# Kernel optimization log

Hardware: AMD Instinct MI355X
Metric: run time of the kernel (lower is better)

The kernel has to match this reference:

```python
import jax, jax.numpy as jnp
import numpy as np

VOCAB = 100000
DIM = 128
B = 16384
C_MAX = 10
K_NEG = 5


def setup_inputs() -> dict:
    key = jax.random.key(0)
    k1, k2, k3, k4, k5, k6 = jax.random.split(key, 6)
    bound = 0.5 / DIM
    return {
        "target_words": jax.random.randint(k1, (B,), 0, VOCAB),
        "context_words": jax.random.randint(k2, (B, C_MAX), 0, VOCAB),
        "context_lens": jax.random.randint(k3, (B,), 0, C_MAX + 1),
        "negative_words": jax.random.randint(k4, (B, K_NEG), 0, VOCAB),
        # input embeddings init: uniform(-0.5/dim, 0.5/dim); output init zeros in the
        # original, but we use small random values so gradients/scores are non-trivial.
        "in_emb": jax.random.uniform(k5, (VOCAB, DIM), jnp.float32, -bound, bound),
        "out_emb": jax.random.normal(k6, (VOCAB, DIM), jnp.float32) * 0.01,
    }


def reference(target_words, context_words, context_lens, negative_words, in_emb, out_emb):
    t = in_emb[target_words]                      # (B, D)
    c = out_emb[context_words]                    # (B, C, D)
    n = out_emb[negative_words]                   # (B, K, D)

    pos_scores = jnp.einsum("bd,bcd->bc", t, c)   # (B, C)
    neg_scores = jnp.einsum("bd,bkd->bk", t, n)   # (B, K)

    mask = (jnp.arange(C_MAX)[None, :] < context_lens[:, None]).astype(t.dtype)
    lens = context_lens.astype(t.dtype)
    has_ctx = lens > 0

    # per-sample mean of -logsigmoid over valid contexts; skip samples with 0 contexts
    pos_per = -jnp.sum(jax.nn.log_sigmoid(pos_scores) * mask, axis=1)
    pos_per = jnp.where(has_ctx, pos_per / jnp.maximum(lens, 1.0), 0.0)

    neg_per = -jnp.mean(jax.nn.log_sigmoid(-neg_scores), axis=1)
    neg_per = jnp.where(has_ctx, neg_per, 0.0)    # original `continue` skips negatives too

    positive_loss = jnp.sum(pos_per) / B
    negative_loss = jnp.sum(neg_per) / B
    return positive_loss, negative_loss
```

## Files before the change

kernel.cpp:

```cpp
#include <hip/hip_runtime.h>
#include <math.h>
#include <stdint.h>

#define VOCAB 100000
#define DIM   128
#define BATCH 16384
#define CMAX  10
#define KNEG  5
#define NSCORE (CMAX + KNEG)
#define JPAD  16

typedef float f32x4 __attribute__((ext_vector_type(4)));

__device__ __forceinline__ float log_sigmoid(float x) {
    return fminf(x, 0.0f) - log1pf(expf(-fabsf(x)));
}

#define DPP_ADD_STEP(v, ctrl)                                                  \
    v += __int_as_float(__builtin_amdgcn_update_dpp(                           \
        0, __float_as_int(v), (ctrl), 0xF, 0xF, false))

__device__ __forceinline__ float dpp_reduce32_to_lane31(float v) {
    DPP_ADD_STEP(v, 0x111);
    DPP_ADD_STEP(v, 0x112);
    DPP_ADD_STEP(v, 0x114);
    DPP_ADD_STEP(v, 0x118);
    DPP_ADD_STEP(v, 0x142);
    return v;
}

__global__ __launch_bounds__(256) void score_kernel(
    const int*   __restrict__ tgt,
    const int*   __restrict__ ctx,
    const int*   __restrict__ neg,
    const float* __restrict__ in_emb,
    const float* __restrict__ out_emb,
    float*       __restrict__ scores,
    float*       __restrict__ out)
{
    const int tid  = threadIdx.x;
    const int sub  = tid & 31;
    const int task = (blockIdx.x * 256 + tid) >> 5;
    const int b    = task >> 2;
    const int g    = task & 3;
    const int j0   = g * 4;

    if (blockIdx.x == 0 && tid < 2) out[tid] = 0.0f;

    const int t_word = tgt[b];
    int words[4];
#pragma unroll
    for (int jj = 0; jj < 4; ++jj) {
        const int j = j0 + jj;
        if (j < CMAX)        words[jj] = ctx[b * CMAX + j];
        else if (j < NSCORE) words[jj] = neg[b * KNEG + (j - CMAX)];
        else                 words[jj] = 0;
    }

    const uint32_t sub16 = (uint32_t)sub * 16u;

    f32x4 tv;
    {
        uint32_t off = (uint32_t)t_word * (DIM * 4u) + sub16;
        asm volatile("global_load_dwordx4 %0, %1, %2"
                     : "=v"(tv) : "v"(off), "s"(in_emb));
    }
    f32x4 rv[4];
#pragma unroll
    for (int jj = 0; jj < 4; ++jj) {
        uint32_t off = (uint32_t)words[jj] * (DIM * 4u) + sub16;
        asm volatile("global_load_dwordx4 %0, %1, %2"
                     : "=v"(rv[jj]) : "v"(off), "s"(out_emb));
    }
    asm volatile("s_waitcnt vmcnt(0)"
                 : "+v"(tv), "+v"(rv[0]), "+v"(rv[1]), "+v"(rv[2]), "+v"(rv[3])
                 :
                 : "memory");

    float p[4];
#pragma unroll
    for (int jj = 0; jj < 4; ++jj) {
        float d = tv.x * rv[jj].x + tv.y * rv[jj].y +
                  tv.z * rv[jj].z + tv.w * rv[jj].w;
        p[jj] = dpp_reduce32_to_lane31(d);
    }

    if (sub == 31) {
        float* s = scores + (size_t)b * JPAD + j0;
#pragma unroll
        for (int jj = 0; jj < 4; ++jj) s[jj] = p[jj];
    }
}

__global__ __launch_bounds__(256) void loss_kernel(
    const float* __restrict__ scores,
    const int*   __restrict__ lens,
    float*       __restrict__ out)
{
    const int tid = threadIdx.x;
    const int b   = blockIdx.x * 256 + tid;

    const int len = lens[b];
    const float* s = scores + (size_t)b * JPAD;

    float sc[NSCORE];
#pragma unroll
    for (int j = 0; j < NSCORE; ++j) sc[j] = s[j];

    float pos_acc = 0.0f;
#pragma unroll
    for (int c = 0; c < CMAX; ++c)
        if (c < len) pos_acc += log_sigmoid(sc[c]);
    float neg_acc = 0.0f;
#pragma unroll
    for (int k = 0; k < KNEG; ++k)
        neg_acc += log_sigmoid(-sc[CMAX + k]);

    float pos_per = 0.0f, neg_per = 0.0f;
    if (len > 0) {
        pos_per = -pos_acc / (float)len;
        neg_per = -neg_acc * (1.0f / KNEG);
    }

#pragma unroll
    for (int m = 32; m >= 1; m >>= 1) {
        pos_per += __shfl_xor(pos_per, m, 64);
        neg_per += __shfl_xor(neg_per, m, 64);
    }
    __shared__ float s_pos[4];
    __shared__ float s_neg[4];
    const int wave = tid >> 6;
    if ((tid & 63) == 0) { s_pos[wave] = pos_per; s_neg[wave] = neg_per; }
    __syncthreads();
    if (tid == 0) {
        float ps = s_pos[0] + s_pos[1] + s_pos[2] + s_pos[3];
        float ns = s_neg[0] + s_neg[1] + s_neg[2] + s_neg[3];
        atomicAdd(&out[0], ps * (1.0f / BATCH));
        atomicAdd(&out[1], ns * (1.0f / BATCH));
    }
}

extern "C" void kernel_launch(void* const* d_in, const int* in_sizes, int n_in,
                              void* d_out, int out_size, void* d_ws, size_t ws_size,
                              hipStream_t stream) {
    const int*   tgt     = (const int*)  d_in[0];
    const int*   ctx     = (const int*)  d_in[1];
    const int*   lens    = (const int*)  d_in[2];
    const int*   neg     = (const int*)  d_in[3];
    const float* in_emb  = (const float*)d_in[4];
    const float* out_emb = (const float*)d_in[5];
    float* out    = (float*)d_out;
    float* scores = (float*)d_ws;

    score_kernel<<<(BATCH * 4) / 8, 256, 0, stream>>>(
        tgt, ctx, neg, in_emb, out_emb, scores, out);

    loss_kernel<<<BATCH / 256, 256, 0, stream>>>(scores, lens, out);
}
```

Baseline: 136.4 us.

## Fuse log-sigmoid loss into score kernel with one wave per sample

Remaps work so one 64-lane wave handles a whole sample: each 32-lane half computes 8 dot products, then the wave broadcasts the scores, applies log-sigmoid and masking, and reduces them in-register. Only a per-sample float2 is written, and a lighter reduce kernel sums it, which removes the 16-float score scratch round-trip. The gather loads are now waited on one at a time with staggered vmcnt so compute overlaps the remaining loads. In exchange, the target row load is per-half instead of shared across more tasks, and there are fewer, larger waves with more registers live per lane.

```diff
diff --git a/kernel.cpp b/kernel.cpp
--- a/kernel.cpp
+++ b/kernel.cpp
@@ -7,8 +7,6 @@
 #define BATCH 16384
 #define CMAX  10
 #define KNEG  5
-#define NSCORE (CMAX + KNEG)
-#define JPAD  16
 
 typedef float f32x4 __attribute__((ext_vector_type(4)));
 
@@ -29,108 +27,127 @@
     return v;
 }
 
-__global__ __launch_bounds__(256) void score_kernel(
+__global__ __launch_bounds__(256) void score_loss_kernel(
     const int*   __restrict__ tgt,
     const int*   __restrict__ ctx,
+    const int*   __restrict__ lens,
     const int*   __restrict__ neg,
     const float* __restrict__ in_emb,
     const float* __restrict__ out_emb,
-    float*       __restrict__ scores,
+    float2*      __restrict__ per_sample,
     float*       __restrict__ out)
 {
     const int tid  = threadIdx.x;
-    const int sub  = tid & 31;
-    const int task = (blockIdx.x * 256 + tid) >> 5;
-    const int b    = task >> 2;
-    const int g    = task & 3;
-    const int j0   = g * 4;
+    const int lane = tid & 63;
+    const int sub  = lane & 31;
+    const int half = lane >> 5;
+    const int b    = (blockIdx.x * 256 + tid) >> 6;
 
     if (blockIdx.x == 0 && tid < 2) out[tid] = 0.0f;
 
+    const int len    = lens[b];
     const int t_word = tgt[b];
-    int words[4];
+    int words[8];
 #pragma unroll
-    for (int jj = 0; jj < 4; ++jj) {
-        const int j = j0 + jj;
-        if (j < CMAX)        words[jj] = ctx[b * CMAX + j];
-        else if (j < NSCORE) words[jj] = neg[b * KNEG + (j - CMAX)];
-        else                 words[jj] = 0;
+    for (int jj = 0; jj < 8; ++jj) {
+        const int j = half * 8 + jj;
+        if (j < CMAX)             words[jj] = ctx[b * CMAX + j];
+        else if (j < CMAX + KNEG) words[jj] = neg[b * KNEG + (j - CMAX)];
+        else                      words[jj] = 0;
     }
 
+    asm volatile("s_waitcnt vmcnt(0)" ::: "memory");
+
     const uint32_t sub16 = (uint32_t)sub * 16u;
-
     f32x4 tv;
     {
         uint32_t off = (uint32_t)t_word * (DIM * 4u) + sub16;
         asm volatile("global_load_dwordx4 %0, %1, %2"
                      : "=v"(tv) : "v"(off), "s"(in_emb));
     }
-    f32x4 rv[4];
+    f32x4 rv[8];
 #pragma unroll
-    for (int jj = 0; jj < 4; ++jj) {
+    for (int jj = 0; jj < 8; ++jj) {
         uint32_t off = (uint32_t)words[jj] * (DIM * 4u) + sub16;
         asm volatile("global_load_dwordx4 %0, %1, %2"
                      : "=v"(rv[jj]) : "v"(off), "s"(out_emb));
     }
-    asm volatile("s_waitcnt vmcnt(0)"
-                 : "+v"(tv), "+v"(rv[0]), "+v"(rv[1]), "+v"(rv[2]), "+v"(rv[3])
-                 :
-                 : "memory");
 
-    float p[4];
+    float p[8];
 #pragma unroll
-    for (int jj = 0; jj < 4; ++jj) {
+    for (int jj = 0; jj < 8; ++jj) {
+        asm volatile("s_waitcnt vmcnt(%[cnt])"
+                     : "+v"(rv[jj]), "+v"(tv)
+                     : [cnt] "i"(7 - jj)
+                     : "memory");
         float d = tv.x * rv[jj].x + tv.y * rv[jj].y +
                   tv.z * rv[jj].z + tv.w * rv[jj].w;
         p[jj] = dpp_reduce32_to_lane31(d);
     }
 
-    if (sub == 31) {
-        float* s = scores + (size_t)b * JPAD + j0;
+    float bc[8];
 #pragma unroll
-        for (int jj = 0; jj < 4; ++jj) s[jj] = p[jj];
+    for (int jj = 0; jj < 8; ++jj) bc[jj] = __shfl(p[jj], 31, 32);
+
+    const int sel = sub & 7;
+    float a0 = (sel & 1) ? bc[1] : bc[0];
+    float a1 = (sel & 1) ? bc[3] : bc[2];
+    float a2 = (sel & 1) ? bc[5] : bc[4];
+    float a3 = (sel & 1) ? bc[7] : bc[6];
+    float b0 = (sel & 2) ? a1 : a0;
+    float b1 = (sel & 2) ? a3 : a2;
+    float s  = (sel & 4) ? b1 : b0;
+
+    const int  j        = half * 8 + sel;
+    const bool neg_slot = (j >= CMAX) && (j < CMAX + KNEG);
+    const bool active   = (sub < 8);
+
+    float v    = log_sigmoid(neg_slot ? -s : s);
+    float posc = (active && j < len)    ? v : 0.0f;
+    float negc = (active && neg_slot)   ? v : 0.0f;
+
+    posc += __shfl_xor(posc, 1, 64);
+    posc += __shfl_xor(posc, 2, 64);
+    posc += __shfl_xor(posc, 4, 64);
+    posc += __shfl_xor(posc, 32, 64);
+    negc += __shfl_xor(negc, 1, 64);
+    negc += __shfl_xor(negc, 2, 64);
+    negc += __shfl_xor(negc, 4, 64);
+    negc += __shfl_xor(negc, 32, 64);
+
+    if (lane == 0) {
+        float2 r;
+        if (len > 0) {
+            r.x = -posc / (float)len;
+            r.y = -negc * (1.0f / KNEG);
+        } else {
+            r.x = 0.0f;
+            r.y = 0.0f;
+        }
+        per_sample[b] = r;
     }
 }
 
-__global__ __launch_bounds__(256) void loss_kernel(
-    const float* __restrict__ scores,
-    const int*   __restrict__ lens,
-    float*       __restrict__ out)
+__global__ __launch_bounds__(256) void reduce_kernel(
+    const float2* __restrict__ per_sample,
+    float*        __restrict__ out)
 {
     const int tid = threadIdx.x;
     const int b   = blockIdx.x * 256 + tid;
 
-    const int len = lens[b];
-    const float* s = scores + (size_t)b * JPAD;
-
-    float sc[NSCORE];
-#pragma unroll
-    for (int j = 0; j < NSCORE; ++j) sc[j] = s[j];
-
-    float pos_acc = 0.0f;
-#pragma unroll
-    for (int c = 0; c < CMAX; ++c)
-        if (c < len) pos_acc += log_sigmoid(sc[c]);
-    float neg_acc = 0.0f;
-#pragma unroll
-    for (int k = 0; k < KNEG; ++k)
-        neg_acc += log_sigmoid(-sc[CMAX + k]);
-
-    float pos_per = 0.0f, neg_per = 0.0f;
-    if (len > 0) {
-        pos_per = -pos_acc / (float)len;
-        neg_per = -neg_acc * (1.0f / KNEG);
-    }
+    const float2 pr = per_sample[b];
+    float pos = pr.x;
+    float neg = pr.y;
 
 #pragma unroll
     for (int m = 32; m >= 1; m >>= 1) {
-        pos_per += __shfl_xor(pos_per, m, 64);
-        neg_per += __shfl_xor(neg_per, m, 64);
+        pos += __shfl_xor(pos, m, 64);
+        neg += __shfl_xor(neg, m, 64);
     }
     __shared__ float s_pos[4];
     __shared__ float s_neg[4];
     const int wave = tid >> 6;
-    if ((tid & 63) == 0) { s_pos[wave] = pos_per; s_neg[wave] = neg_per; }
+    if ((tid & 63) == 0) { s_pos[wave] = pos; s_neg[wave] = neg; }
     __syncthreads();
     if (tid == 0) {
         float ps = s_pos[0] + s_pos[1] + s_pos[2] + s_pos[3];
@@ -149,11 +166,11 @@
     const int*   neg     = (const int*)  d_in[3];
     const float* in_emb  = (const float*)d_in[4];
     const float* out_emb = (const float*)d_in[5];
-    float* out    = (float*)d_out;
-    float* scores = (float*)d_ws;
+    float* out          = (float*)d_out;
+    float2* per_sample  = (float2*)d_ws;
 
-    score_kernel<<<(BATCH * 4) / 8, 256, 0, stream>>>(
-        tgt, ctx, neg, in_emb, out_emb, scores, out);
+    score_loss_kernel<<<BATCH / 4, 256, 0, stream>>>(
+        tgt, ctx, lens, neg, in_emb, out_emb, per_sample, out);
 
-    loss_kernel<<<BATCH / 256, 256, 0, stream>>>(scores, lens, out);
+    reduce_kernel<<<BATCH / 256, 256, 0, stream>>>(per_sample, out);
 }
```

Result: faster. 132.0 us (-3.2%).
